# Performance work log

Measured on AMD Instinct MI355X. Metric: run time of the kernel, lower is better.

The kernel has to match this reference:

```python
import jax, jax.numpy as jnp
import numpy as np

_LN2 = 0.6931471805599453
B, N, C, R, K = 256, 4096, 256, 32, 128
MAX_SPAN = 20.0
W_WEIGHT, W_COACT, W_SPAN = 1.0, 1.0, 0.3


def setup_inputs() -> dict:
    key = jax.random.key(0)
    k1, k2, k3, k4, k5 = jax.random.split(key, 5)
    A = jax.random.normal(k1, (B, N), dtype=jnp.float32)            # accumulated atom activations
    span_t = jax.random.uniform(k2, (B,), dtype=jnp.float32) * MAX_SPAN
    proto_weights = jax.random.normal(k3, (C, N), dtype=jnp.float32) * 0.5
    proto_coact_U = jax.random.normal(k4, (C, N, R), dtype=jnp.float32) * 0.1
    proto_span = jax.random.normal(k5, (C,), dtype=jnp.float32) + 5.0
    return {"A": A, "span_t": span_t, "proto_weights": proto_weights,
            "proto_coact_U": proto_coact_U, "proto_span": proto_span}


def reference(A, span_t, proto_weights, proto_coact_U, proto_span):
    # CoActivationComputer._compute: top-K atoms per trajectory
    topk_vals, topk_idx = jax.lax.top_k(A, K)                       # [B,K], [B,K]

    # --- match_score ---
    proto_w = jax.nn.softplus(proto_weights) - _LN2                 # [C,N]
    score_w = A @ proto_w.T                                          # [B,C]
    score_w = score_w - jnp.mean(score_w, axis=1, keepdims=True)

    # CoActState.frob_inner_lowrank: gather U rows at top-k indices
    U_t = jnp.transpose(proto_coact_U, (1, 2, 0))                    # [N,R,C]
    U_topk = U_t[topk_idx]                                           # [B,K,R,C] (irregular gather)
    Au = jnp.einsum('bk,bkrc->brc', topk_vals, U_topk)               # [B,R,C]
    score_coact = jnp.sum(Au ** 2, axis=1) / (K * R + 1e-9)          # [B,C]

    span_norm = jnp.clip(span_t / MAX_SPAN, 0.0, 1.0)                # [B]
    proto_span_norm = jax.nn.sigmoid(proto_span)                     # [C]
    score_span = -jnp.abs(span_norm[:, None] - proto_span_norm[None, :])

    match_scores = W_WEIGHT * score_w + W_COACT * score_coact + W_SPAN * score_span  # [B,C]

    # --- compute_residual_score ---
    beta = jax.nn.softmax(match_scores, axis=-1)                     # [B,C]
    U_recon = jnp.einsum('bc,cnr->bnr', beta, proto_coact_U)         # [B,N,R]
    norm_Mhat = jnp.sum(topk_vals ** 2, axis=1)                      # [B]
    U_recon_topk = jnp.take_along_axis(U_recon, topk_idx[:, :, None], axis=1)  # [B,K,R]
    Au2 = jnp.einsum('bk,bkr->br', topk_vals, U_recon_topk)          # [B,R]
    cross = jnp.sum(Au2 ** 2, axis=1) / (K * R + 1e-9)
    norm_Mrecon = jnp.sum(U_recon ** 2, axis=(1, 2)) / (K * R + 1e-9)
    norm_Mhat_n = norm_Mhat / (K + 1e-9)
    residual = jnp.clip(norm_Mhat_n - 2.0 * cross + norm_Mrecon, 0.0, 10000.0)  # [B]
    return residual
```

## Files before the change

### kernel.cpp

```cpp
#include <hip/hip_runtime.h>
#include <math.h>

#define Bb 256
#define Nn 4096
#define Cc 256
#define Rr 32
#define Kk 128
#define Lflat (Nn * Rr)
#define LN2f 0.6931471805599453f
#define SKW 16

typedef unsigned short u16;
typedef __attribute__((ext_vector_type(8))) short short8b;
typedef __attribute__((ext_vector_type(4))) short short4b;
typedef __attribute__((ext_vector_type(4))) float f32x4;

typedef __attribute__((address_space(1))) const void* gas_t;
typedef __attribute__((address_space(3))) void* las_t;
__device__ __forceinline__ void gll16(const void* g, void* l) {
  __builtin_amdgcn_global_load_lds((gas_t)g, (las_t)l, 16, 0, 0);
}

__device__ inline u16 f2bf(float x) {
  unsigned u = __float_as_uint(x);
  unsigned r = (u + 0x7fffu + ((u >> 16) & 1u)) >> 16;
  return (u16)r;
}

__device__ inline unsigned f2u(float f) {
  unsigned b = __float_as_uint(f);
  return (b & 0x80000000u) ? ~b : (b | 0x80000000u);
}
__device__ inline float u2f(unsigned u) {
  unsigned b = (u & 0x80000000u) ? (u ^ 0x80000000u) : ~u;
  return __uint_as_float(b);
}

__global__ __launch_bounds__(256) void topk_kernel(const float* __restrict__ A,
                                                   int* __restrict__ tidx,
                                                   float* __restrict__ tval) {
  __shared__ unsigned su[Nn];
  __shared__ int s_cnt;
  __shared__ int s_eqidx[256];
  __shared__ int s_eqcnt;
  int b = blockIdx.x, t = threadIdx.x;
  const float* row = A + (size_t)b * Nn;
  for (int i = t; i < Nn; i += 256) su[i] = f2u(row[i]);
  __syncthreads();
  unsigned T = 0u;
  for (int bit = 31; bit >= 0; --bit) {
    unsigned cand = T | (1u << bit);
    int local = 0;
    for (int i = t; i < Nn; i += 256) local += (su[i] >= cand) ? 1 : 0;
#pragma unroll
    for (int off = 32; off; off >>= 1) local += __shfl_down(local, off, 64);
    __syncthreads();
    if (t == 0) s_cnt = 0;
    __syncthreads();
    if ((t & 63) == 0) atomicAdd(&s_cnt, local);
    __syncthreads();
    if (s_cnt >= Kk) T = cand;
  }
  __syncthreads();
  if (t == 0) { s_cnt = 0; s_eqcnt = 0; }
  __syncthreads();
  for (int i = t; i < Nn; i += 256) {
    unsigned u = su[i];
    if (u > T) {
      int p = atomicAdd(&s_cnt, 1);
      tidx[b * Kk + p] = i;
      tval[b * Kk + p] = u2f(u);
    } else if (u == T) {
      int p = atomicAdd(&s_eqcnt, 1);
      if (p < 256) s_eqidx[p] = i;
    }
  }
  __syncthreads();
  int m = s_cnt;
  int eq = min(s_eqcnt, 256);
  if (t == 0) {
    float tv = u2f(T);
    for (int s = m; s < Kk; ++s) {
      int best = 0x7fffffff, bi = 0;
      for (int j = 0; j < eq; ++j)
        if (s_eqidx[j] < best) { best = s_eqidx[j]; bi = j; }
      tidx[b * Kk + s] = best;
      tval[b * Kk + s] = tv;
      s_eqidx[bi] = 0x7fffffff;
    }
  }
}

__global__ __launch_bounds__(256) void scatter_kernel(const int* __restrict__ tidx,
                                                      const float* __restrict__ tval,
                                                      u16* __restrict__ S) {
  int b = blockIdx.x, t = threadIdx.x;
  short8b z = {0, 0, 0, 0, 0, 0, 0, 0};
  u16* row = S + (size_t)b * Nn;
  *(short8b*)(row + t * 16) = z;
  *(short8b*)(row + t * 16 + 8) = z;
  __syncthreads();
  if (t < Kk) row[tidx[b * Kk + t]] = f2bf(tval[b * Kk + t]);
}

__global__ __launch_bounds__(256) void u2t_kernel(const float* __restrict__ U,
                                                  u16* __restrict__ UT) {
  int c = blockIdx.x, nb = blockIdx.y, t = threadIdx.x;
  __shared__ u16 B16[64 * 32];
  const float* Uc = U + (size_t)c * Lflat;
  u16* UTc = UT + (size_t)c * Lflat;
  for (int it = 0; it < 8; ++it) {
    int n0 = nb * 512 + it * 64;
    __syncthreads();
    for (int u = t; u < 512; u += 256) {
      int n = u >> 3, rq = u & 7;
      float4 f = *(const float4*)(Uc + (size_t)(n0 + n) * Rr + rq * 4);
      union { short4b v; u16 s[4]; } pk;
      pk.s[0] = f2bf(f.x); pk.s[1] = f2bf(f.y); pk.s[2] = f2bf(f.z); pk.s[3] = f2bf(f.w);
      *(short4b*)(&B16[n * 32 + rq * 4]) = pk.v;
    }
    __syncthreads();
    {
      int r = t >> 3, q = t & 7;
      union { short8b v; u16 s[8]; } pk;
#pragma unroll
      for (int i = 0; i < 8; ++i) pk.s[i] = B16[(q * 8 + i) * 32 + r];
      *(short8b*)(UTc + (size_t)r * Nn + n0 + q * 8) = pk.v;
    }
  }
}

__global__ __launch_bounds__(256) void scorew_mfma_kernel(const float* __restrict__ Ag,
                                                          const float* __restrict__ W,
                                                          float* __restrict__ SWp) {
  int ct = blockIdx.x, mt = blockIdx.y, ks = blockIdx.z;
  int t = threadIdx.x;
  int lane = t & 63, wave = t >> 6;
  int lo = lane & 15, hi = lane >> 4;
  int wr = wave >> 1, wc = wave & 1;
  __shared__ __align__(16) u16 As[64 * 64];
  __shared__ __align__(16) u16 Ws[64 * 64];
  f32x4 acc[2][2];
#pragma unroll
  for (int m = 0; m < 2; ++m)
#pragma unroll
    for (int n = 0; n < 2; ++n) acc[m][n] = (f32x4){0.f, 0.f, 0.f, 0.f};
  int kbase = ks * (Nn / SKW);
  for (int k0 = 0; k0 < Nn / SKW; k0 += 64) {
    for (int s = t; s < 1024; s += 256) {
      int panel = s >> 9;
      int sl = s & 511;
      int row = sl >> 3, q = sl & 7;
      union { short8b v; u16 u[8]; } pk;
      if (panel == 0) {
        const float* src = Ag + (size_t)(mt * 64 + row) * Nn + kbase + k0 + q * 8;
        float4 f0 = *(const float4*)src, f1 = *(const float4*)(src + 4);
        pk.u[0] = f2bf(f0.x); pk.u[1] = f2bf(f0.y); pk.u[2] = f2bf(f0.z); pk.u[3] = f2bf(f0.w);
        pk.u[4] = f2bf(f1.x); pk.u[5] = f2bf(f1.y); pk.u[6] = f2bf(f1.z); pk.u[7] = f2bf(f1.w);
        *(short8b*)(&As[row * 64 + ((q ^ (row & 7)) << 3)]) = pk.v;
      } else {
        const float* src = W + (size_t)(ct * 64 + row) * Nn + kbase + k0 + q * 8;
        float4 f0 = *(const float4*)src, f1 = *(const float4*)(src + 4);
        float w[8] = {f0.x, f0.y, f0.z, f0.w, f1.x, f1.y, f1.z, f1.w};
#pragma unroll
        for (int j = 0; j < 8; ++j)
          pk.u[j] = f2bf(fmaxf(w[j], 0.f) + log1pf(expf(-fabsf(w[j]))) - LN2f);
        *(short8b*)(&Ws[row * 64 + ((q ^ (row & 7)) << 3)]) = pk.v;
      }
    }
    __syncthreads();
#pragma unroll
    for (int kf = 0; kf < 2; ++kf) {
      int q = kf * 4 + hi;
      short8b af[2], bf[2];
#pragma unroll
      for (int m = 0; m < 2; ++m) {
        int row = wr * 32 + m * 16 + lo;
        af[m] = *(const short8b*)(&As[row * 64 + ((q ^ (row & 7)) << 3)]);
      }
#pragma unroll
      for (int n = 0; n < 2; ++n) {
        int row = wc * 32 + n * 16 + lo;
        bf[n] = *(const short8b*)(&Ws[row * 64 + ((q ^ (row & 7)) << 3)]);
      }
#pragma unroll
      for (int m = 0; m < 2; ++m)
#pragma unroll
        for (int n = 0; n < 2; ++n)
          acc[m][n] = __builtin_amdgcn_mfma_f32_16x16x32_bf16(af[m], bf[n], acc[m][n], 0, 0, 0);
    }
    __syncthreads();
  }
  float* o = SWp + (size_t)ks * (Bb * Cc);
#pragma unroll
  for (int m = 0; m < 2; ++m)
#pragma unroll
    for (int n = 0; n < 2; ++n)
#pragma unroll
      for (int r = 0; r < 4; ++r) {
        int b = mt * 64 + wr * 32 + m * 16 + hi * 4 + r;
        int c = ct * 64 + wc * 32 + n * 16 + lo;
        o[(size_t)b * Cc + c] = acc[m][n][r];
      }
}

__global__ __launch_bounds__(256) void gram_bf16_kernel(const u16* __restrict__ UT,
                                                        float* __restrict__ Gpart,
                                                        int kch) {
  int bx = blockIdx.x;
  int tile = bx % 3, chunk = bx / 3;
  int ti = (tile == 2) ? 1 : 0;
  int tj = (tile == 0) ? 0 : 1;
  bool diag = (tile != 1);
  int t = threadIdx.x, lane = t & 63, wave = t >> 6;
  int lo = lane & 15, hi = lane >> 4;
  int wr = wave >> 1, wc = wave & 1;
  __shared__ __align__(16) u16 lp[2][128 * 64];
  f32x4 acc[4][4];
#pragma unroll
  for (int m = 0; m < 4; ++m)
#pragma unroll
    for (int n = 0; n < 4; ++n) acc[m][n] = (f32x4){0.f, 0.f, 0.f, 0.f};
  int lrow = lane >> 3;
  int lchunk8 = ((lane & 7) ^ lrow) * 8;
  size_t kbase = (size_t)chunk * kch;
  for (int k0 = 0; k0 < kch; k0 += 64) {
    size_t kg = kbase + k0;
#pragma unroll
    for (int q = 0; q < 4; ++q) {
      int row = wave * 32 + q * 8;
      gll16(UT + (size_t)(ti * 128 + row + lrow) * Lflat + kg + lchunk8, &lp[0][row * 64]);
    }
    if (!diag) {
#pragma unroll
      for (int q = 0; q < 4; ++q) {
        int row = wave * 32 + q * 8;
        gll16(UT + (size_t)(tj * 128 + row + lrow) * Lflat + kg + lchunk8, &lp[1][row * 64]);
      }
    }
    __syncthreads();
#pragma unroll
    for (int ks = 0; ks < 2; ++ks) {
      short8b af[4], bfv[4];
#pragma unroll
      for (int m = 0; m < 4; ++m) {
        int row = wr * 64 + m * 16 + lo;
        af[m] = *(const short8b*)(&lp[0][row * 64 + (((ks * 4 + hi) ^ (row & 7)) << 3)]);
      }
      const u16* pb = diag ? lp[0] : lp[1];
#pragma unroll
      for (int n = 0; n < 4; ++n) {
        int row = wc * 64 + n * 16 + lo;
        bfv[n] = *(const short8b*)(&pb[row * 64 + (((ks * 4 + hi) ^ (row & 7)) << 3)]);
      }
#pragma unroll
      for (int m = 0; m < 4; ++m)
#pragma unroll
        for (int n = 0; n < 4; ++n)
          acc[m][n] = __builtin_amdgcn_mfma_f32_16x16x32_bf16(af[m], bfv[n], acc[m][n], 0, 0, 0);
    }
    __syncthreads();
  }
  float* gp = Gpart + (size_t)bx * 16384;
#pragma unroll
  for (int m = 0; m < 4; ++m)
#pragma unroll
    for (int n = 0; n < 4; ++n)
#pragma unroll
      for (int r = 0; r < 4; ++r) {
        int row = wr * 64 + m * 16 + hi * 4 + r;
        int col = wc * 64 + n * 16 + lo;
        gp[row * 128 + col] = acc[m][n][r];
      }
}

__global__ __launch_bounds__(256) void gram_mfma_kernel(const float* __restrict__ U,
                                                        float* __restrict__ Gpart,
                                                        int kch) {
  int bx = blockIdx.x;
  int tile = bx % 3;
  int chunk = bx / 3;
  int ti = (tile == 2) ? 1 : 0;
  int tj = (tile == 0) ? 0 : 1;
  bool diag = (tile != 1);
  int t = threadIdx.x;
  int lane = t & 63, wave = t >> 6;
  int lo = lane & 15, hi = lane >> 4;
  int wr = wave >> 1, wc = wave & 1;
  __shared__ __align__(16) u16 lp[2][128 * 64];
  size_t kbase = (size_t)chunk * kch;
  f32x4 acc[4][4];
#pragma unroll
  for (int m = 0; m < 4; ++m)
#pragma unroll
    for (int n = 0; n < 4; ++n) acc[m][n] = (f32x4){0.f, 0.f, 0.f, 0.f};
  int nslots = diag ? 1024 : 2048;
  for (int k0 = 0; k0 < kch; k0 += 64) {
    for (int s = t; s < nslots; s += 256) {
      int panel = s >> 10;
      int sl = s & 1023;
      int row = sl >> 3, q = sl & 7;
      int grow = (panel ? tj : ti) * 128 + row;
      const float* src = U + (size_t)grow * Lflat + kbase + k0 + q * 8;
      float4 f0 = *(const float4*)src;
      float4 f1 = *(const float4*)(src + 4);
      union { short8b v; u16 u[8]; } pk;
      pk.u[0] = f2bf(f0.x); pk.u[1] = f2bf(f0.y); pk.u[2] = f2bf(f0.z); pk.u[3] = f2bf(f0.w);
      pk.u[4] = f2bf(f1.x); pk.u[5] = f2bf(f1.y); pk.u[6] = f2bf(f1.z); pk.u[7] = f2bf(f1.w);
      *(short8b*)(&lp[panel][row * 64 + ((q ^ (row & 7)) << 3)]) = pk.v;
    }
    __syncthreads();
#pragma unroll
    for (int ks = 0; ks < 2; ++ks) {
      short8b af[4], bfv[4];
#pragma unroll
      for (int m = 0; m < 4; ++m) {
        int row = wr * 64 + m * 16 + lo;
        af[m] = *(const short8b*)(&lp[0][row * 64 + (((ks * 4 + hi) ^ (row & 7)) << 3)]);
      }
      const u16* pb = diag ? lp[0] : lp[1];
#pragma unroll
      for (int n = 0; n < 4; ++n) {
        int row = wc * 64 + n * 16 + lo;
        bfv[n] = *(const short8b*)(&pb[row * 64 + (((ks * 4 + hi) ^ (row & 7)) << 3)]);
      }
#pragma unroll
      for (int m = 0; m < 4; ++m)
#pragma unroll
        for (int n = 0; n < 4; ++n)
          acc[m][n] = __builtin_amdgcn_mfma_f32_16x16x32_bf16(af[m], bfv[n], acc[m][n], 0, 0, 0);
    }
    __syncthreads();
  }
  float* gp = Gpart + (size_t)bx * 16384;
#pragma unroll
  for (int m = 0; m < 4; ++m)
#pragma unroll
    for (int n = 0; n < 4; ++n)
#pragma unroll
      for (int r = 0; r < 4; ++r) {
        int row = wr * 64 + m * 16 + hi * 4 + r;
        int col = wc * 64 + n * 16 + lo;
        gp[row * 128 + col] = acc[m][n][r];
      }
}

__global__ __launch_bounds__(256) void gram_reduce_kernel(const float* __restrict__ Gpart,
                                                          float* __restrict__ G,
                                                          int nchunks) {
  int tile = blockIdx.x % 3, seg = blockIdx.x / 3;
  int ti = (tile == 2) ? 1 : 0;
  int tj = (tile == 0) ? 0 : 1;
  int e = seg * 1024 + threadIdx.x * 4;
  float4 s = {0.f, 0.f, 0.f, 0.f};
  for (int ch = 0; ch < nchunks; ++ch) {
    float4 v = *(const float4*)(Gpart + ((size_t)(ch * 3 + tile)) * 16384 + e);
    s.x += v.x; s.y += v.y; s.z += v.z; s.w += v.w;
  }
  int row = e >> 7, col = e & 127;
  int gi = ti * 128 + row, gj = tj * 128 + col;
  G[gi * Cc + gj + 0] = s.x;
  G[gi * Cc + gj + 1] = s.y;
  G[gi * Cc + gj + 2] = s.z;
  G[gi * Cc + gj + 3] = s.w;
  if (tile == 1) {
    G[(gj + 0) * Cc + gi] = s.x;
    G[(gj + 1) * Cc + gi] = s.y;
    G[(gj + 2) * Cc + gi] = s.z;
    G[(gj + 3) * Cc + gi] = s.w;
  }
}

__global__ __launch_bounds__(256) void au_gemm_kernel(const u16* __restrict__ S,
                                                      const u16* __restrict__ UT,
                                                      float* __restrict__ Au,
                                                      float* __restrict__ SC) {
  int jt = blockIdx.x, bt = blockIdx.y;
  int t = threadIdx.x, lane = t & 63, wave = t >> 6;
  int lo = lane & 15, hi = lane >> 4;
  int wr = wave >> 1, wc = wave & 1;
  __shared__ __align__(16) u16 Sa[128 * 64];
  __shared__ __align__(16) u16 Ub[64 * 64];
  f32x4 acc[4][2];
#pragma unroll
  for (int m = 0; m < 4; ++m)
#pragma unroll
    for (int n = 0; n < 2; ++n) acc[m][n] = (f32x4){0.f, 0.f, 0.f, 0.f};
  int lrow = lane >> 3;
  int lchunk8 = ((lane & 7) ^ lrow) * 8;
  for (int k0 = 0; k0 < Nn; k0 += 64) {
#pragma unroll
    for (int q = 0; q < 4; ++q) {
      int row = wave * 32 + q * 8;
      gll16(S + (size_t)(bt * 128 + row + lrow) * Nn + k0 + lchunk8, &Sa[row * 64]);
    }
#pragma unroll
    for (int q = 0; q < 2; ++q) {
      int row = wave * 16 + q * 8;
      gll16(UT + (size_t)(jt * 64 + row + lrow) * Nn + k0 + lchunk8, &Ub[row * 64]);
    }
    __syncthreads();
#pragma unroll
    for (int ks = 0; ks < 2; ++ks) {
      int q = ks * 4 + hi;
      short8b af[4], bfv[2];
#pragma unroll
      for (int m = 0; m < 4; ++m) {
        int r = wr * 64 + m * 16 + lo;
        af[m] = *(const short8b*)(&Sa[r * 64 + ((q ^ (r & 7)) << 3)]);
      }
#pragma unroll
      for (int n = 0; n < 2; ++n) {
        int r = wc * 32 + n * 16 + lo;
        bfv[n] = *(const short8b*)(&Ub[r * 64 + ((q ^ (r & 7)) << 3)]);
      }
#pragma unroll
      for (int m = 0; m < 4; ++m)
#pragma unroll
        for (int n = 0; n < 2; ++n)
          acc[m][n] = __builtin_amdgcn_mfma_f32_16x16x32_bf16(af[m], bfv[n], acc[m][n], 0, 0, 0);
    }
    __syncthreads();
  }
  int c = jt * 2 + wc;
#pragma unroll
  for (int m = 0; m < 4; ++m)
#pragma unroll
    for (int rr = 0; rr < 4; ++rr) {
      int b = bt * 128 + wr * 64 + m * 16 + hi * 4 + rr;
      float a0 = acc[m][0][rr], a1 = acc[m][1][rr];
      Au[((size_t)b * Cc + c) * Rr + lo]      = a0;
      Au[((size_t)b * Cc + c) * Rr + 16 + lo] = a1;
      float sq = a0 * a0 + a1 * a1;
      sq += __shfl_xor(sq, 1, 64);
      sq += __shfl_xor(sq, 2, 64);
      sq += __shfl_xor(sq, 4, 64);
      sq += __shfl_xor(sq, 8, 64);
      if (lo == 0) SC[(size_t)b * Cc + c] = sq * (1.f / (Kk * Rr));
    }
}

__global__ __launch_bounds__(256) void au_mfma_kernel(const float* __restrict__ U,
                                                      const u16* __restrict__ S,
                                                      float* __restrict__ Au,
                                                      float* __restrict__ SC) {
  int c = blockIdx.x, mb = blockIdx.y;
  int t = threadIdx.x;
  int lane = t & 63, wave = t >> 6;
  int lo = lane & 15, hi = lane >> 4;
  __shared__ __align__(16) u16 Ss[128 * 64];
  __shared__ __align__(16) u16 Us[32 * 64];
  f32x4 acc[2][2];
#pragma unroll
  for (int m = 0; m < 2; ++m)
#pragma unroll
    for (int n = 0; n < 2; ++n) acc[m][n] = (f32x4){0.f, 0.f, 0.f, 0.f};
  const float* Uc = U + (size_t)c * Lflat;
  for (int k0 = 0; k0 < Nn; k0 += 64) {
    for (int s = t; s < 1024; s += 256) {
      int row = s >> 3, q = s & 7;
      short8b v = *(const short8b*)(S + (size_t)(mb * 128 + row) * Nn + k0 + q * 8);
      *(short8b*)(&Ss[row * 64 + ((q ^ (row & 7)) << 3)]) = v;
    }
    for (int s = t; s < 512; s += 256) {
      int kk = s >> 3, rq = s & 7;
      float4 f = *(const float4*)(Uc + (size_t)(k0 + kk) * Rr + rq * 4);
      float fv[4] = {f.x, f.y, f.z, f.w};
#pragma unroll
      for (int j = 0; j < 4; ++j) {
        int r = rq * 4 + j;
        Us[r * 64 + (((kk >> 3) ^ (r & 7)) << 3) + (kk & 7)] = f2bf(fv[j]);
      }
    }
    __syncthreads();
#pragma unroll
    for (int kf = 0; kf < 2; ++kf) {
      int q = kf * 4 + hi;
      short8b af[2], bf[2];
#pragma unroll
      for (int m = 0; m < 2; ++m) {
        int row = wave * 32 + m * 16 + lo;
        af[m] = *(const short8b*)(&Ss[row * 64 + ((q ^ (row & 7)) << 3)]);
      }
#pragma unroll
      for (int n = 0; n < 2; ++n) {
        int row = n * 16 + lo;
        bf[n] = *(const short8b*)(&Us[row * 64 + ((q ^ (row & 7)) << 3)]);
      }
#pragma unroll
      for (int m = 0; m < 2; ++m)
#pragma unroll
        for (int n = 0; n < 2; ++n)
          acc[m][n] = __builtin_amdgcn_mfma_f32_16x16x32_bf16(af[m], bf[n], acc[m][n], 0, 0, 0);
    }
    __syncthreads();
  }
#pragma unroll
  for (int m = 0; m < 2; ++m) {
#pragma unroll
    for (int r = 0; r < 4; ++r) {
      int b = mb * 128 + wave * 32 + m * 16 + hi * 4 + r;
#pragma unroll
      for (int n = 0; n < 2; ++n) {
        int rr = n * 16 + lo;
        Au[((size_t)b * Cc + c) * Rr + rr] = acc[m][n][r];
      }
      float sq = acc[m][0][r] * acc[m][0][r] + acc[m][1][r] * acc[m][1][r];
      sq += __shfl_xor(sq, 1, 64);
      sq += __shfl_xor(sq, 2, 64);
      sq += __shfl_xor(sq, 4, 64);
      sq += __shfl_xor(sq, 8, 64);
      if (lo == 0) SC[(size_t)b * Cc + c] = sq * (1.f / (Kk * Rr));
    }
  }
}

__global__ __launch_bounds__(256) void softmax_kernel(const float* __restrict__ SWp,
                                                      const float* __restrict__ SC,
                                                      const float* __restrict__ span_t,
                                                      const float* __restrict__ PS,
                                                      float* __restrict__ beta) {
  int b = blockIdx.x, t = threadIdx.x;
  float span_norm = fminf(fmaxf(span_t[b] * (1.f / 20.f), 0.f), 1.f);
  float psn = 1.f / (1.f + expf(-PS[t]));
  float m = 0.f;
#pragma unroll
  for (int kc = 0; kc < SKW; ++kc) m += SWp[(size_t)kc * (Bb * Cc) + b * Cc + t];
  m += SC[b * Cc + t] - 0.3f * fabsf(span_norm - psn);
  __shared__ float redM[4], redS[4];
  float mx = m;
#pragma unroll
  for (int off = 32; off; off >>= 1) mx = fmaxf(mx, __shfl_xor(mx, off, 64));
  if ((t & 63) == 0) redM[t >> 6] = mx;
  __syncthreads();
  mx = fmaxf(fmaxf(redM[0], redM[1]), fmaxf(redM[2], redM[3]));
  float e = expf(m - mx);
  float s = e;
#pragma unroll
  for (int off = 32; off; off >>= 1) s += __shfl_xor(s, off, 64);
  if ((t & 63) == 0) redS[t >> 6] = s;
  __syncthreads();
  s = redS[0] + redS[1] + redS[2] + redS[3];
  beta[b * Cc + t] = e / s;
}

__global__ __launch_bounds__(256) void final_kernel(const float* __restrict__ beta,
                                                    const float* __restrict__ G,
                                                    const float* __restrict__ Au,
                                                    const float* __restrict__ tval,
                                                    float* __restrict__ out) {
  int b = blockIdx.x, t = threadIdx.x;
  __shared__ float sb[Cc];
  __shared__ float au2[8][32];
  __shared__ float redA[4], redB[4];
  sb[t] = beta[b * Cc + t];
  __syncthreads();
  float w = 0.f;
  for (int c = 0; c < Cc; ++c) w = fmaf(sb[c], G[c * Cc + t], w);
  float pr = sb[t] * w;
  int r = t & 31, g = t >> 5;
  float p = 0.f;
#pragma unroll 8
  for (int cc = 0; cc < 32; ++cc) {
    int c = cc * 8 + g;
    p = fmaf(sb[c], Au[((size_t)b * Cc + c) * Rr + r], p);
  }
  au2[g][r] = p;
  float h = (t < Kk) ? tval[b * Kk + t] * tval[b * Kk + t] : 0.f;
  float x = pr;
#pragma unroll
  for (int off = 32; off; off >>= 1) x += __shfl_xor(x, off, 64);
  if ((t & 63) == 0) redA[t >> 6] = x;
  float y = h;
#pragma unroll
  for (int off = 32; off; off >>= 1) y += __shfl_xor(y, off, 64);
  if ((t & 63) == 0) redB[t >> 6] = y;
  __syncthreads();
  float recon = (redA[0] + redA[1] + redA[2] + redA[3]) * (1.f / 4096.f);
  float mhat  = (redB[0] + redB[1] + redB[2] + redB[3]) * (1.f / 128.f);
  float cr = 0.f;
  if (t < 32) {
    float a2 = 0.f;
#pragma unroll
    for (int gg = 0; gg < 8; ++gg) a2 += au2[gg][t];
    cr = a2 * a2;
  }
#pragma unroll
  for (int off = 16; off; off >>= 1) cr += __shfl_xor(cr, off, 64);
  if (t == 0) {
    cr *= (1.f / 4096.f);
    float res = mhat - 2.f * cr + recon;
    res = fminf(fmaxf(res, 0.f), 10000.f);
    out[b] = res;
  }
}

extern "C" void kernel_launch(void* const* d_in, const int* in_sizes, int n_in,
                              void* d_out, int out_size, void* d_ws, size_t ws_size,
                              hipStream_t stream) {
  const float* A      = (const float*)d_in[0];
  const float* span_t = (const float*)d_in[1];
  const float* W      = (const float*)d_in[2];
  const float* U      = (const float*)d_in[3];
  const float* PS     = (const float*)d_in[4];
  float* out = (float*)d_out;

  char* p = (char*)d_ws;
  int*   tidx = (int*)p;   p += (size_t)Bb * Kk * 4;
  float* tval = (float*)p; p += (size_t)Bb * Kk * 4;
  float* SWp  = (float*)p; p += (size_t)SKW * Bb * Cc * 4;
  float* SC   = (float*)p; p += (size_t)Bb * Cc * 4;
  float* beta = (float*)p; p += (size_t)Bb * Cc * 4;
  float* G    = (float*)p; p += (size_t)Cc * Cc * 4;
  u16*   S    = (u16*)p;   p += (size_t)Bb * Nn * 2;
  float* Au   = (float*)p; p += (size_t)Bb * Cc * Rr * 4;
  size_t fixed = (size_t)(p - (char*)d_ws);
  size_t UTsz = (size_t)Cc * Lflat * 2;
  bool planA = ws_size >= fixed + UTsz + (size_t)3 * 8 * 16384 * 4;

  topk_kernel<<<dim3(Bb), dim3(256), 0, stream>>>(A, tidx, tval);
  scatter_kernel<<<dim3(Bb), dim3(256), 0, stream>>>(tidx, tval, S);
  scorew_mfma_kernel<<<dim3(4, 4, SKW), dim3(256), 0, stream>>>(A, W, SWp);

  if (planA) {
    u16* UT = (u16*)p; p += UTsz;
    size_t used = fixed + UTsz;
    int nchunks = 64;
    while (nchunks > 8 && used + (size_t)(3 * nchunks) * 16384 * 4 > ws_size) nchunks >>= 1;
    float* Gpart = (float*)p;
    u2t_kernel<<<dim3(Cc, 8), dim3(256), 0, stream>>>(U, UT);
    gram_bf16_kernel<<<dim3(3 * nchunks), dim3(256), 0, stream>>>(UT, Gpart, Lflat / nchunks);
    gram_reduce_kernel<<<dim3(48), dim3(256), 0, stream>>>(Gpart, G, nchunks);
    au_gemm_kernel<<<dim3(128, 2), dim3(256), 0, stream>>>(S, UT, Au, SC);
  } else {
    int nchunks = 64;
    while (nchunks > 8 && fixed + (size_t)(3 * nchunks) * 16384 * 4 > ws_size) nchunks >>= 1;
    float* Gpart = (float*)p;
    gram_mfma_kernel<<<dim3(3 * nchunks), dim3(256), 0, stream>>>(U, Gpart, Lflat / nchunks);
    gram_reduce_kernel<<<dim3(48), dim3(256), 0, stream>>>(Gpart, G, nchunks);
    au_mfma_kernel<<<dim3(Cc, 2), dim3(256), 0, stream>>>(U, S, Au, SC);
  }

  softmax_kernel<<<dim3(Bb), dim3(256), 0, stream>>>(SWp, SC, span_t, PS, beta);
  final_kernel<<<dim3(Bb), dim3(256), 0, stream>>>(beta, G, Au, tval, out);
}
```

Baseline: 211.7 us.

## Radix-select top-k fused with scatter, simplify transpose, fuse softmax and final

Replaces the 32-pass bitwise threshold search in top-k with a 4-pass 8-bit radix histogram select held in registers. The kernel now writes the sparse bf16 row and the squared-norm sum directly, which removes the separate scatter kernel and the tidx/tval buffers. The U transpose drops its shared-memory staging in favour of direct strided reads, and softmax is fused with the final residual kernel so beta never goes through global memory. The strided transpose reads may coalesce worse, and the top-k depends on per-wave shared atomics.

Result: faster. 193.3 us, median of 4 (-8.7%).

```diff
diff --git a/kernel.cpp b/kernel.cpp
--- a/kernel.cpp
+++ b/kernel.cpp
@@ -12,7 +12,6 @@
 
 typedef unsigned short u16;
 typedef __attribute__((ext_vector_type(8))) short short8b;
-typedef __attribute__((ext_vector_type(4))) short short4b;
 typedef __attribute__((ext_vector_type(4))) float f32x4;
 
 typedef __attribute__((address_space(1))) const void* gas_t;
@@ -37,96 +36,110 @@
 }
 
 __global__ __launch_bounds__(256) void topk_kernel(const float* __restrict__ A,
-                                                   int* __restrict__ tidx,
-                                                   float* __restrict__ tval) {
-  __shared__ unsigned su[Nn];
-  __shared__ int s_cnt;
+                                                   u16* __restrict__ S,
+                                                   float* __restrict__ mhat) {
+  int b = blockIdx.x, t = threadIdx.x;
+  int lane = t & 63, wave = t >> 6;
+  const float* row = A + (size_t)b * Nn;
+  u16* Srow = S + (size_t)b * Nn;
+  short8b z = {0, 0, 0, 0, 0, 0, 0, 0};
+  *(short8b*)(Srow + t * 16) = z;
+  *(short8b*)(Srow + t * 16 + 8) = z;
+
+  float f[16]; unsigned u[16];
+#pragma unroll
+  for (int j = 0; j < 4; ++j) {
+    float4 v = ((const float4*)row)[j * 256 + t];
+    f[j * 4 + 0] = v.x; f[j * 4 + 1] = v.y; f[j * 4 + 2] = v.z; f[j * 4 + 3] = v.w;
+  }
+#pragma unroll
+  for (int j = 0; j < 16; ++j) u[j] = f2u(f[j]);
+
+  __shared__ int hist[4][256];
+  __shared__ int sufs[257];
+  __shared__ int wtot[4];
+  __shared__ int s_d, s_cg;
   __shared__ int s_eqidx[256];
   __shared__ int s_eqcnt;
-  int b = blockIdx.x, t = threadIdx.x;
-  const float* row = A + (size_t)b * Nn;
-  for (int i = t; i < Nn; i += 256) su[i] = f2u(row[i]);
+  __shared__ float redQ[4];
+  if (t == 0) s_eqcnt = 0;
+
+  unsigned T = 0u;
+  int cntG = 0;
+#pragma unroll
+  for (int p = 3; p >= 0; --p) {
+    hist[0][t] = 0; hist[1][t] = 0; hist[2][t] = 0; hist[3][t] = 0;
+    __syncthreads();
+    unsigned mh = (p == 3) ? 0u : (0xFFFFFFFFu << (8 * (p + 1)));
+    int* hw = hist[wave];
+#pragma unroll
+    for (int j = 0; j < 16; ++j)
+      if (((u[j] ^ T) & mh) == 0) atomicAdd(&hw[(u[j] >> (8 * p)) & 255], 1);
+    __syncthreads();
+    int v = hist[0][t] + hist[1][t] + hist[2][t] + hist[3][t];
+#pragma unroll
+    for (int off = 1; off < 64; off <<= 1) {
+      int tmp = __shfl_down(v, off, 64);
+      if (lane + off < 64) v += tmp;
+    }
+    if (lane == 0) wtot[wave] = v;
+    __syncthreads();
+    for (int w2 = wave + 1; w2 < 4; ++w2) v += wtot[w2];
+    sufs[t] = v;
+    if (t == 0) sufs[256] = 0;
+    __syncthreads();
+    int nxt = sufs[t + 1];
+    if ((cntG + v >= Kk) && (cntG + nxt < Kk)) { s_d = t; s_cg = cntG + nxt; }
+    __syncthreads();
+    T |= (unsigned)s_d << (8 * p);
+    cntG = s_cg;
+    __syncthreads();
+  }
+  float sq = 0.f;
+#pragma unroll
+  for (int j = 0; j < 16; ++j) {
+    int idx = (j >> 2) * 1024 + t * 4 + (j & 3);
+    if (u[j] > T) {
+      Srow[idx] = f2bf(f[j]);
+      sq += f[j] * f[j];
+    } else if (u[j] == T) {
+      int q2 = atomicAdd(&s_eqcnt, 1);
+      if (q2 < 256) s_eqidx[q2] = idx;
+    }
+  }
+#pragma unroll
+  for (int off = 32; off; off >>= 1) sq += __shfl_xor(sq, off, 64);
+  if (lane == 0) redQ[wave] = sq;
   __syncthreads();
-  unsigned T = 0u;
-  for (int bit = 31; bit >= 0; --bit) {
-    unsigned cand = T | (1u << bit);
-    int local = 0;
-    for (int i = t; i < Nn; i += 256) local += (su[i] >= cand) ? 1 : 0;
-#pragma unroll
-    for (int off = 32; off; off >>= 1) local += __shfl_down(local, off, 64);
-    __syncthreads();
-    if (t == 0) s_cnt = 0;
-    __syncthreads();
-    if ((t & 63) == 0) atomicAdd(&s_cnt, local);
-    __syncthreads();
-    if (s_cnt >= Kk) T = cand;
-  }
-  __syncthreads();
-  if (t == 0) { s_cnt = 0; s_eqcnt = 0; }
-  __syncthreads();
-  for (int i = t; i < Nn; i += 256) {
-    unsigned u = su[i];
-    if (u > T) {
-      int p = atomicAdd(&s_cnt, 1);
-      tidx[b * Kk + p] = i;
-      tval[b * Kk + p] = u2f(u);
-    } else if (u == T) {
-      int p = atomicAdd(&s_eqcnt, 1);
-      if (p < 256) s_eqidx[p] = i;
-    }
-  }
-  __syncthreads();
-  int m = s_cnt;
-  int eq = min(s_eqcnt, 256);
   if (t == 0) {
     float tv = u2f(T);
-    for (int s = m; s < Kk; ++s) {
+    u16 tb = f2bf(tv);
+    int need = Kk - cntG;
+    int eq = min(s_eqcnt, 256);
+    for (int s2 = 0; s2 < need; ++s2) {
       int best = 0x7fffffff, bi = 0;
-      for (int j = 0; j < eq; ++j)
-        if (s_eqidx[j] < best) { best = s_eqidx[j]; bi = j; }
-      tidx[b * Kk + s] = best;
-      tval[b * Kk + s] = tv;
+      for (int jj = 0; jj < eq; ++jj)
+        if (s_eqidx[jj] < best) { best = s_eqidx[jj]; bi = jj; }
+      Srow[best] = tb;
       s_eqidx[bi] = 0x7fffffff;
     }
-  }
-}
-
-__global__ __launch_bounds__(256) void scatter_kernel(const int* __restrict__ tidx,
-                                                      const float* __restrict__ tval,
-                                                      u16* __restrict__ S) {
-  int b = blockIdx.x, t = threadIdx.x;
-  short8b z = {0, 0, 0, 0, 0, 0, 0, 0};
-  u16* row = S + (size_t)b * Nn;
-  *(short8b*)(row + t * 16) = z;
-  *(short8b*)(row + t * 16 + 8) = z;
-  __syncthreads();
-  if (t < Kk) row[tidx[b * Kk + t]] = f2bf(tval[b * Kk + t]);
+    mhat[b] = redQ[0] + redQ[1] + redQ[2] + redQ[3] + (float)need * tv * tv;
+  }
 }
 
 __global__ __launch_bounds__(256) void u2t_kernel(const float* __restrict__ U,
                                                   u16* __restrict__ UT) {
   int c = blockIdx.x, nb = blockIdx.y, t = threadIdx.x;
-  __shared__ u16 B16[64 * 32];
+  int r = t & 31, nblk = t >> 5;
   const float* Uc = U + (size_t)c * Lflat;
   u16* UTc = UT + (size_t)c * Lflat;
   for (int it = 0; it < 8; ++it) {
-    int n0 = nb * 512 + it * 64;
-    __syncthreads();
-    for (int u = t; u < 512; u += 256) {
-      int n = u >> 3, rq = u & 7;
-      float4 f = *(const float4*)(Uc + (size_t)(n0 + n) * Rr + rq * 4);
-      union { short4b v; u16 s[4]; } pk;
-      pk.s[0] = f2bf(f.x); pk.s[1] = f2bf(f.y); pk.s[2] = f2bf(f.z); pk.s[3] = f2bf(f.w);
-      *(short4b*)(&B16[n * 32 + rq * 4]) = pk.v;
-    }
-    __syncthreads();
-    {
-      int r = t >> 3, q = t & 7;
-      union { short8b v; u16 s[8]; } pk;
-#pragma unroll
-      for (int i = 0; i < 8; ++i) pk.s[i] = B16[(q * 8 + i) * 32 + r];
-      *(short8b*)(UTc + (size_t)r * Nn + n0 + q * 8) = pk.v;
-    }
+    int n0 = nb * 512 + it * 64 + nblk * 8;
+    union { short8b v; u16 s[8]; } pk;
+#pragma unroll
+    for (int i = 0; i < 8; ++i)
+      pk.s[i] = f2bf(Uc[(size_t)(n0 + i) * Rr + r]);
+    *(short8b*)(UTc + (size_t)r * Nn + n0) = pk.v;
   }
 }
 
@@ -515,83 +528,71 @@
   }
 }
 
-__global__ __launch_bounds__(256) void softmax_kernel(const float* __restrict__ SWp,
+__global__ __launch_bounds__(256) void softfin_kernel(const float* __restrict__ SWp,
                                                       const float* __restrict__ SC,
                                                       const float* __restrict__ span_t,
                                                       const float* __restrict__ PS,
-                                                      float* __restrict__ beta) {
+                                                      const float* __restrict__ G,
+                                                      const float* __restrict__ Au,
+                                                      const float* __restrict__ mhat,
+                                                      float* __restrict__ out) {
   int b = blockIdx.x, t = threadIdx.x;
+  int lane = t & 63, wave = t >> 6;
+  __shared__ float redM[4], redS[4], redA[4];
+  __shared__ float sb[Cc];
+  __shared__ float au2[8][32];
   float span_norm = fminf(fmaxf(span_t[b] * (1.f / 20.f), 0.f), 1.f);
   float psn = 1.f / (1.f + expf(-PS[t]));
   float m = 0.f;
 #pragma unroll
   for (int kc = 0; kc < SKW; ++kc) m += SWp[(size_t)kc * (Bb * Cc) + b * Cc + t];
   m += SC[b * Cc + t] - 0.3f * fabsf(span_norm - psn);
-  __shared__ float redM[4], redS[4];
   float mx = m;
 #pragma unroll
   for (int off = 32; off; off >>= 1) mx = fmaxf(mx, __shfl_xor(mx, off, 64));
-  if ((t & 63) == 0) redM[t >> 6] = mx;
+  if (lane == 0) redM[wave] = mx;
   __syncthreads();
   mx = fmaxf(fmaxf(redM[0], redM[1]), fmaxf(redM[2], redM[3]));
   float e = expf(m - mx);
   float s = e;
 #pragma unroll
   for (int off = 32; off; off >>= 1) s += __shfl_xor(s, off, 64);
-  if ((t & 63) == 0) redS[t >> 6] = s;
+  if (lane == 0) redS[wave] = s;
   __syncthreads();
   s = redS[0] + redS[1] + redS[2] + redS[3];
-  beta[b * Cc + t] = e / s;
-}
-
-__global__ __launch_bounds__(256) void final_kernel(const float* __restrict__ beta,
-                                                    const float* __restrict__ G,
-                                                    const float* __restrict__ Au,
-                                                    const float* __restrict__ tval,
-                                                    float* __restrict__ out) {
-  int b = blockIdx.x, t = threadIdx.x;
-  __shared__ float sb[Cc];
-  __shared__ float au2[8][32];
-  __shared__ float redA[4], redB[4];
-  sb[t] = beta[b * Cc + t];
+  float beta_t = e / s;
+  sb[t] = beta_t;
   __syncthreads();
   float w = 0.f;
+#pragma unroll 8
   for (int c = 0; c < Cc; ++c) w = fmaf(sb[c], G[c * Cc + t], w);
-  float pr = sb[t] * w;
+  float pr = beta_t * w;
   int r = t & 31, g = t >> 5;
-  float p = 0.f;
+  float pp = 0.f;
 #pragma unroll 8
   for (int cc = 0; cc < 32; ++cc) {
     int c = cc * 8 + g;
-    p = fmaf(sb[c], Au[((size_t)b * Cc + c) * Rr + r], p);
-  }
-  au2[g][r] = p;
-  float h = (t < Kk) ? tval[b * Kk + t] * tval[b * Kk + t] : 0.f;
+    pp = fmaf(sb[c], Au[((size_t)b * Cc + c) * Rr + r], pp);
+  }
+  au2[g][r] = pp;
   float x = pr;
 #pragma unroll
   for (int off = 32; off; off >>= 1) x += __shfl_xor(x, off, 64);
-  if ((t & 63) == 0) redA[t >> 6] = x;
-  float y = h;
-#pragma unroll
-  for (int off = 32; off; off >>= 1) y += __shfl_xor(y, off, 64);
-  if ((t & 63) == 0) redB[t >> 6] = y;
+  if (lane == 0) redA[wave] = x;
   __syncthreads();
   float recon = (redA[0] + redA[1] + redA[2] + redA[3]) * (1.f / 4096.f);
-  float mhat  = (redB[0] + redB[1] + redB[2] + redB[3]) * (1.f / 128.f);
   float cr = 0.f;
   if (t < 32) {
-    float a2 = 0.f;
-#pragma unroll
-    for (int gg = 0; gg < 8; ++gg) a2 += au2[gg][t];
+    float a2 = au2[0][t] + au2[1][t] + au2[2][t] + au2[3][t]
+             + au2[4][t] + au2[5][t] + au2[6][t] + au2[7][t];
     cr = a2 * a2;
   }
 #pragma unroll
   for (int off = 16; off; off >>= 1) cr += __shfl_xor(cr, off, 64);
   if (t == 0) {
     cr *= (1.f / 4096.f);
-    float res = mhat - 2.f * cr + recon;
-    res = fminf(fmaxf(res, 0.f), 10000.f);
-    out[b] = res;
+    float res = mhat[b] * (1.f / 128.f) - 2.f * cr + recon;
+    out[b] = fminf(fmaxf(res, 0.f), 10000.f);
   }
 }
 
@@ -606,11 +607,9 @@
   float* out = (float*)d_out;
 
   char* p = (char*)d_ws;
-  int*   tidx = (int*)p;   p += (size_t)Bb * Kk * 4;
-  float* tval = (float*)p; p += (size_t)Bb * Kk * 4;
+  float* mhat = (float*)p; p += (size_t)Bb * 4;
   float* SWp  = (float*)p; p += (size_t)SKW * Bb * Cc * 4;
   float* SC   = (float*)p; p += (size_t)Bb * Cc * 4;
-  float* beta = (float*)p; p += (size_t)Bb * Cc * 4;
   float* G    = (float*)p; p += (size_t)Cc * Cc * 4;
   u16*   S    = (u16*)p;   p += (size_t)Bb * Nn * 2;
   float* Au   = (float*)p; p += (size_t)Bb * Cc * Rr * 4;
@@ -618,8 +617,7 @@
   size_t UTsz = (size_t)Cc * Lflat * 2;
   bool planA = ws_size >= fixed + UTsz + (size_t)3 * 8 * 16384 * 4;
 
-  topk_kernel<<<dim3(Bb), dim3(256), 0, stream>>>(A, tidx, tval);
-  scatter_kernel<<<dim3(Bb), dim3(256), 0, stream>>>(tidx, tval, S);
+  topk_kernel<<<dim3(Bb), dim3(256), 0, stream>>>(A, S, mhat);
   scorew_mfma_kernel<<<dim3(4, 4, SKW), dim3(256), 0, stream>>>(A, W, SWp);
 
   if (planA) {
@@ -641,6 +639,5 @@
     au_mfma_kernel<<<dim3(Cc, 2), dim3(256), 0, stream>>>(U, S, Au, SC);
   }
 
-  softmax_kernel<<<dim3(Bb), dim3(256), 0, stream>>>(SWp, SC, span_t, PS, beta);
-  final_kernel<<<dim3(Bb), dim3(256), 0, stream>>>(beta, G, Au, tval, out);
-}
+  softfin_kernel<<<dim3(Bb), dim3(256), 0, stream>>>(SWp, SC, span_t, PS, G, Au, mhat, out);
+}
```
